# Optimization experiments

Measured on AMD Instinct MI355X. Metric: run time of the kernel, lower is better.

## Reference

```python
import jax, jax.numpy as jnp
import numpy as np

B, TQ, TK = 4, 256, 256
Q, K, H = 256, 256, 256


def setup_inputs() -> dict:
    key = jax.random.key(0)
    ks = jax.random.split(key, 10)
    s = 0.05
    return {
        "queries": jax.random.normal(ks[0], (B, TQ, Q), dtype=jnp.float32),
        "keys": jax.random.normal(ks[1], (B, TK, K), dtype=jnp.float32),
        # lengths in [T//2, T] so no fully-masked query rows (torch would NaN there too)
        "query_lengths": jax.random.randint(ks[2], (B,), TQ // 2, TQ + 1),
        "key_lengths": jax.random.randint(ks[3], (B,), TK // 2, TK + 1),
        # nn.Linear(Q+K, H): weight applied as x @ W1; torch concat order is [keys, queries]
        "W1": jax.random.normal(ks[4], (K + Q, H), dtype=jnp.float32) * s,
        "b1": jax.random.normal(ks[5], (H,), dtype=jnp.float32) * s,
        "W2": jax.random.normal(ks[6], (H, H), dtype=jnp.float32) * s,
        "b2": jax.random.normal(ks[7], (H,), dtype=jnp.float32) * s,
        "W3": jax.random.normal(ks[8], (H, 1), dtype=jnp.float32) * s,
        "b3": jax.random.normal(ks[9], (1,), dtype=jnp.float32) * s,
    }


def reference(queries, keys, query_lengths, key_lengths, W1, b1, W2, b2, W3, b3):
    Bn, Tq, Qd = queries.shape
    Tk, Kd = keys.shape[1], keys.shape[2]
    # Split the first linear: concat([keys, queries]) @ W1 == keys@W1[:K] + queries@W1[K:]
    kh = jnp.einsum("bkd,dh->bkh", keys, W1[:Kd])      # [B,Tk,H]
    qh = jnp.einsum("bqd,dh->bqh", queries, W1[Kd:])   # [B,Tq,H]
    h = jax.nn.relu(qh[:, :, None, :] + kh[:, None, :, :] + b1)  # [B,Tq,Tk,H]
    h = jax.nn.relu(jnp.einsum("bqkh,hg->bqkg", h, W2) + b2)     # [B,Tq,Tk,H]
    scores = jnp.einsum("bqkh,h->bqk", h, W3[:, 0]) + b3[0]       # [B,Tq,Tk]
    # mask True where position is padding (query OR key out of range)
    mask = (jnp.arange(Tq)[None, :, None] >= query_lengths[:, None, None]) | (
        jnp.arange(Tk)[None, None, :] >= key_lengths[:, None, None]
    )
    scores = jnp.where(mask, -1e30, scores)
    probs = jax.nn.softmax(scores, axis=-1)
    probs = jnp.where(mask, 0.0, probs)
    return jnp.einsum("bqk,bkd->bqd", probs, keys)  # [B,Tq,K]
```

## Files before the change

### kernel.cpp

```cpp
#include <hip/hip_runtime.h>
#include <cstdint>

#define BATCH 4
#define TQ 256
#define TK 256
#define DIM 256
#define HD 256

typedef _Float16 f16x8 __attribute__((ext_vector_type(8)));
typedef float f32x4 __attribute__((ext_vector_type(4)));

union U4H8 { uint4 u; f16x8 v; };

__device__ __forceinline__ unsigned short f2h(float f) {
    _Float16 h = (_Float16)f;
    unsigned short u;
    __builtin_memcpy(&u, &h, 2);
    return u;
}

__device__ __forceinline__ float h2f(unsigned short u) {
    _Float16 h;
    __builtin_memcpy(&h, &u, 2);
    return (float)h;
}

__device__ __forceinline__ uint32_t pk2h(float a, float b) {
    auto r = __builtin_amdgcn_cvt_pkrtz(a, b);
    uint32_t w;
    __builtin_memcpy(&w, &r, 4);
    return w;
}

__global__ __launch_bounds__(256) void pack(
    const float* __restrict__ queries, const float* __restrict__ keys,
    const float* __restrict__ W1, const float* __restrict__ W2,
    unsigned short* __restrict__ Xh, unsigned short* __restrict__ Xl,
    unsigned short* __restrict__ W1Th, unsigned short* __restrict__ W1Tl,
    unsigned short* __restrict__ W2T) {
    int i = blockIdx.x;
    int t = threadIdx.x;
    if (i < 512) {
        const float* src = (i < 256 ? queries : keys) + (((i & 255) * 256 + t) << 2);
        float4 v = *(const float4*)src;
        uint32_t h0 = pk2h(v.x, v.y), h1 = pk2h(v.z, v.w);
        float f0 = h2f((unsigned short)h0), f1 = h2f((unsigned short)(h0 >> 16));
        float f2 = h2f((unsigned short)h1), f3 = h2f((unsigned short)(h1 >> 16));
        uint32_t l0 = pk2h(v.x - f0, v.y - f1), l1 = pk2h(v.z - f2, v.w - f3);
        int o = i * 256 + t;
        ((uint2*)Xh)[o] = make_uint2(h0, h1);
        ((uint2*)Xl)[o] = make_uint2(l0, l1);
        return;
    }
    __shared__ float tile[32][33];
    int tx = t & 31, ty = t >> 5;
    if (i < 640) {
        int bi = i - 512;
        int kt = (bi >> 3) * 32, nt = (bi & 7) * 32;
#pragma unroll
        for (int r = 0; r < 4; ++r)
            tile[ty + r * 8][tx] = W1[(kt + ty + r * 8) * HD + nt + tx];
        __syncthreads();
#pragma unroll
        for (int r = 0; r < 4; ++r) {
            float v = tile[tx][ty + r * 8];
            unsigned short h = f2h(v);
            int o = (nt + ty + r * 8) * 512 + kt + tx;
            W1Th[o] = h;
            W1Tl[o] = f2h(v - h2f(h));
        }
        return;
    }
    int bi = i - 640;
    int tc = (bi & 7) * 32, tn = (bi >> 3) * 32;
#pragma unroll
    for (int r = 0; r < 4; ++r)
        tile[ty + r * 8][tx] = W2[(tc + ty + r * 8) * HD + tn + tx];
    __syncthreads();
#pragma unroll
    for (int r = 0; r < 4; ++r)
        W2T[(tn + ty + r * 8) * HD + tc + tx] = f2h(tile[tx][ty + r * 8]);
}

__global__ __launch_bounds__(256) void prep_mfma(
    const unsigned short* __restrict__ Xh, const unsigned short* __restrict__ Xl,
    const unsigned short* __restrict__ W1Th, const unsigned short* __restrict__ W1Tl,
    const float* __restrict__ b1, float* __restrict__ qkh) {
    int mblk = blockIdx.x >> 2, nblk = blockIdx.x & 3;
    int t = threadIdx.x, wid = t >> 6, lane = t & 63;
    int col = lane & 15, quad = lane >> 4;
    int arow = mblk * 64 + wid * 16 + col;
    bool isQ = mblk < 16;
    int koff = isQ ? 256 : 0;

    const uint4* axh = (const uint4*)(Xh + arow * DIM) + quad;
    const uint4* axl = (const uint4*)(Xl + arow * DIM) + quad;
    const uint4* pbh[4];
    const uint4* pbl[4];
    float b1v[4];
#pragma unroll
    for (int nt = 0; nt < 4; ++nt) {
        int n = nblk * 64 + nt * 16 + col;
        pbh[nt] = (const uint4*)(W1Th + n * 512 + koff) + quad;
        pbl[nt] = (const uint4*)(W1Tl + n * 512 + koff) + quad;
        b1v[nt] = isQ ? b1[n] : 0.f;
    }
    f32x4 acc[4] = {};
#pragma unroll
    for (int s = 0; s < 8; ++s) {
        U4H8 ah, al;
        ah.u = axh[s * 4];
        al.u = axl[s * 4];
#pragma unroll
        for (int nt = 0; nt < 4; ++nt) {
            U4H8 bh, bl;
            bh.u = pbh[nt][s * 4];
            bl.u = pbl[nt][s * 4];
            acc[nt] = __builtin_amdgcn_mfma_f32_16x16x32_f16(ah.v, bh.v, acc[nt], 0, 0, 0);
            acc[nt] = __builtin_amdgcn_mfma_f32_16x16x32_f16(al.v, bh.v, acc[nt], 0, 0, 0);
            acc[nt] = __builtin_amdgcn_mfma_f32_16x16x32_f16(ah.v, bl.v, acc[nt], 0, 0, 0);
        }
    }
#pragma unroll
    for (int nt = 0; nt < 4; ++nt)
#pragma unroll
        for (int r = 0; r < 4; ++r)
            qkh[(mblk * 64 + wid * 16 + quad * 4 + r) * HD + nblk * 64 + nt * 16 + col] =
                acc[nt][r] + b1v[nt];
}

__global__ __launch_bounds__(256, 3) void mlp_attn(
    const float* __restrict__ qh, const float* __restrict__ kh,
    const unsigned short* __restrict__ W2T,
    const float* __restrict__ b2, const float* __restrict__ W3,
    const float* __restrict__ keys,
    const int* __restrict__ qlens, const int* __restrict__ klens,
    float* __restrict__ out) {
    int bid = blockIdx.x;
    int b = bid >> 8;
    int q = bid & 255;
    int t = threadIdx.x;
    float* orow = out + (b * TQ + q) * DIM;
    if (q >= qlens[b]) { orow[t] = 0.f; return; }
    int klen = klens[b];
    int nch = (klen + 63) >> 6;

    __shared__ uint4 Afrag[8][4][64];
    __shared__ float srow[TK];
    __shared__ float red[8];

    int wid = t >> 6, lane = t & 63;
    int col = lane & 15, quad = lane >> 4;

    int nb = wid * 64;
    const uint4* w2r[4];
    float b2v[4], w3v[4];
#pragma unroll
    for (int nt = 0; nt < 4; ++nt) {
        int n = nb + nt * 16 + col;
        w2r[nt] = (const uint4*)(W2T + n * HD) + quad;
        b2v[nt] = b2[n];
        w3v[nt] = W3[n];
    }

    int p = (wid << 4) | col;
    const float* qrow = qh + (b * TQ + q) * HD + quad * 8;
    const float* kbase = kh + (b * TK) * HD + quad * 8;

    srow[t] = 0.f;

    for (int c = 0; c < nch; ++c) {
        if (c) __syncthreads();
        {
            const float* krow = kbase + (c * 64 + p) * HD;
            uint4* dst = &Afrag[0][wid][lane];
#pragma unroll 2
            for (int s = 0; s < 8; ++s) {
                const float4 k0 = *(const float4*)(krow + s * 32);
                const float4 k1 = *(const float4*)(krow + s * 32 + 4);
                const float4 q0 = *(const float4*)(qrow + s * 32);
                const float4 q1 = *(const float4*)(qrow + s * 32 + 4);
                uint4 w;
                w.x = pk2h(fmaxf(k0.x + q0.x, 0.f), fmaxf(k0.y + q0.y, 0.f));
                w.y = pk2h(fmaxf(k0.z + q0.z, 0.f), fmaxf(k0.w + q0.w, 0.f));
                w.z = pk2h(fmaxf(k1.x + q1.x, 0.f), fmaxf(k1.y + q1.y, 0.f));
                w.w = pk2h(fmaxf(k1.z + q1.z, 0.f), fmaxf(k1.w + q1.w, 0.f));
                dst[s * 256] = w;
            }
        }
        __syncthreads();

        f32x4 acc[4][4] = {};
        uint4 bst[2][4];
#pragma unroll
        for (int nt = 0; nt < 4; ++nt) bst[0][nt] = w2r[nt][0];
#pragma unroll
        for (int s = 0; s < 8; ++s) {
            int pp = s & 1;
            if (s < 7) {
#pragma unroll
                for (int nt = 0; nt < 4; ++nt)
                    bst[pp ^ 1][nt] = w2r[nt][(s + 1) * 4];
            }
#pragma unroll
            for (int mt = 0; mt < 4; ++mt) {
                U4H8 au;
                au.u = Afrag[s][mt][lane];
#pragma unroll
                for (int nt = 0; nt < 4; ++nt) {
                    U4H8 bu;
                    bu.u = bst[pp][nt];
                    acc[mt][nt] = __builtin_amdgcn_mfma_f32_16x16x32_f16(
                        au.v, bu.v, acc[mt][nt], 0, 0, 0);
                }
            }
        }

#pragma unroll
        for (int mt = 0; mt < 4; ++mt) {
            float part[4];
#pragma unroll
            for (int r = 0; r < 4; ++r) {
                float pa = 0.f;
#pragma unroll
                for (int nt = 0; nt < 4; ++nt)
                    pa = fmaf(fmaxf(acc[mt][nt][r] + b2v[nt], 0.f), w3v[nt], pa);
                part[r] = pa;
            }
#pragma unroll
            for (int off = 1; off < 16; off <<= 1)
#pragma unroll
                for (int r = 0; r < 4; ++r)
                    part[r] += __shfl_xor(part[r], off, 64);
            if (col == 0)
#pragma unroll
                for (int r = 0; r < 4; ++r)
                    atomicAdd(&srow[c * 64 + mt * 16 + quad * 4 + r], part[r]);
        }
    }
    __syncthreads();

    float s = (t < klen) ? srow[t] : -3.4e38f;
    float m = s;
#pragma unroll
    for (int off = 1; off < 64; off <<= 1) m = fmaxf(m, __shfl_xor(m, off, 64));
    if (lane == 0) red[wid] = m;
    __syncthreads();
    m = fmaxf(fmaxf(red[0], red[1]), fmaxf(red[2], red[3]));
    float e = (t < klen) ? __expf(s - m) : 0.f;
    float sum = e;
#pragma unroll
    for (int off = 1; off < 64; off <<= 1) sum += __shfl_xor(sum, off, 64);
    if (lane == 0) red[4 + wid] = sum;
    __syncthreads();
    float denom = red[4] + red[5] + red[6] + red[7];
    srow[t] = e / denom;
    __syncthreads();

    float acc = 0.f;
    const float* kp = keys + b * TK * DIM + t;
#pragma unroll 16
    for (int k = 0; k < klen; ++k) acc = fmaf(srow[k], kp[k * DIM], acc);
    orow[t] = acc;
}

extern "C" void kernel_launch(void* const* d_in, const int* in_sizes, int n_in,
                              void* d_out, int out_size, void* d_ws, size_t ws_size,
                              hipStream_t stream) {
    (void)in_sizes; (void)n_in; (void)out_size; (void)ws_size;
    const float* queries = (const float*)d_in[0];
    const float* keys    = (const float*)d_in[1];
    const int*   qlens   = (const int*)d_in[2];
    const int*   klens   = (const int*)d_in[3];
    const float* W1      = (const float*)d_in[4];
    const float* b1      = (const float*)d_in[5];
    const float* W2      = (const float*)d_in[6];
    const float* b2      = (const float*)d_in[7];
    const float* W3      = (const float*)d_in[8];
    float* out = (float*)d_out;

    float* qkh = (float*)d_ws;
    float* qh = qkh;
    float* kh = qkh + 1024 * HD;
    unsigned short* Xh   = (unsigned short*)(qkh + 2048 * HD);
    unsigned short* Xl   = Xh + 2048 * DIM;
    unsigned short* W1Th = Xl + 2048 * DIM;
    unsigned short* W1Tl = W1Th + 256 * 512;
    unsigned short* W2T  = W1Tl + 256 * 512;

    pack<<<704, 256, 0, stream>>>(queries, keys, W1, W2, Xh, Xl, W1Th, W1Tl, W2T);
    prep_mfma<<<128, 256, 0, stream>>>(Xh, Xl, W1Th, W1Tl, b1, qkh);
    mlp_attn<<<BATCH * TQ, 256, 0, stream>>>(
        qh, kh, W2T, b2, W3, keys, qlens, klens, out);
}
```

Before: 153.9 us.

## Split MLP scoring and P·V into separate kernels with wider blocks

The fused per-query kernel is split in two. The first kernel computes the masked softmax probabilities with 512-thread blocks: each wave now covers 32 output columns of W2 instead of 64, and the A-fragment fill is spread across twice as many waves. Probabilities are written to workspace. A second kernel computes probs·keys for four query rows per block, so each key element read is reused four times. The intent is higher MFMA occupancy and less redundant key traffic, at the cost of an extra launch and a round trip of the probability matrix through global memory.

```diff
diff --git a/kernel.cpp b/kernel.cpp
--- a/kernel.cpp
+++ b/kernel.cpp
@@ -129,57 +129,56 @@
                 acc[nt][r] + b1v[nt];
 }
 
-__global__ __launch_bounds__(256, 3) void mlp_attn(
+__global__ __launch_bounds__(512, 4) void mlp_scores(
     const float* __restrict__ qh, const float* __restrict__ kh,
     const unsigned short* __restrict__ W2T,
     const float* __restrict__ b2, const float* __restrict__ W3,
-    const float* __restrict__ keys,
     const int* __restrict__ qlens, const int* __restrict__ klens,
-    float* __restrict__ out) {
+    float* __restrict__ probs) {
     int bid = blockIdx.x;
     int b = bid >> 8;
     int q = bid & 255;
     int t = threadIdx.x;
-    float* orow = out + (b * TQ + q) * DIM;
-    if (q >= qlens[b]) { orow[t] = 0.f; return; }
+    if (q >= qlens[b]) return;
     int klen = klens[b];
     int nch = (klen + 63) >> 6;
 
     __shared__ uint4 Afrag[8][4][64];
     __shared__ float srow[TK];
-    __shared__ float red[8];
-
-    int wid = t >> 6, lane = t & 63;
+    __shared__ float redm[8], reds[8];
+
+    int wv = t >> 6, lane = t & 63;
     int col = lane & 15, quad = lane >> 4;
 
-    int nb = wid * 64;
-    const uint4* w2r[4];
-    float b2v[4], w3v[4];
-#pragma unroll
-    for (int nt = 0; nt < 4; ++nt) {
-        int n = nb + nt * 16 + col;
+    const uint4* w2r[2];
+    float b2v[2], w3v[2];
+#pragma unroll
+    for (int nt = 0; nt < 2; ++nt) {
+        int n = wv * 32 + nt * 16 + col;
         w2r[nt] = (const uint4*)(W2T + n * HD) + quad;
         b2v[nt] = b2[n];
         w3v[nt] = W3[n];
     }
 
-    int p = (wid << 4) | col;
+    int mt_s = wv & 3, s0 = (wv >> 2) << 2;
+    int p = (mt_s << 4) | col;
     const float* qrow = qh + (b * TQ + q) * HD + quad * 8;
     const float* kbase = kh + (b * TK) * HD + quad * 8;
 
-    srow[t] = 0.f;
+    if (t < TK) srow[t] = 0.f;
 
     for (int c = 0; c < nch; ++c) {
         if (c) __syncthreads();
         {
             const float* krow = kbase + (c * 64 + p) * HD;
-            uint4* dst = &Afrag[0][wid][lane];
+            uint4* dst = &Afrag[s0][mt_s][lane];
 #pragma unroll 2
-            for (int s = 0; s < 8; ++s) {
-                const float4 k0 = *(const float4*)(krow + s * 32);
-                const float4 k1 = *(const float4*)(krow + s * 32 + 4);
-                const float4 q0 = *(const float4*)(qrow + s * 32);
-                const float4 q1 = *(const float4*)(qrow + s * 32 + 4);
+            for (int s = 0; s < 4; ++s) {
+                int c0 = (s0 + s) * 32;
+                const float4 k0 = *(const float4*)(krow + c0);
+                const float4 k1 = *(const float4*)(krow + c0 + 4);
+                const float4 q0 = *(const float4*)(qrow + c0);
+                const float4 q1 = *(const float4*)(qrow + c0 + 4);
                 uint4 w;
                 w.x = pk2h(fmaxf(k0.x + q0.x, 0.f), fmaxf(k0.y + q0.y, 0.f));
                 w.y = pk2h(fmaxf(k0.z + q0.z, 0.f), fmaxf(k0.w + q0.w, 0.f));
@@ -190,16 +189,16 @@
         }
         __syncthreads();
 
-        f32x4 acc[4][4] = {};
-        uint4 bst[2][4];
-#pragma unroll
-        for (int nt = 0; nt < 4; ++nt) bst[0][nt] = w2r[nt][0];
+        f32x4 acc[4][2] = {};
+        uint4 bst[2][2];
+#pragma unroll
+        for (int nt = 0; nt < 2; ++nt) bst[0][nt] = w2r[nt][0];
 #pragma unroll
         for (int s = 0; s < 8; ++s) {
             int pp = s & 1;
             if (s < 7) {
 #pragma unroll
-                for (int nt = 0; nt < 4; ++nt)
+                for (int nt = 0; nt < 2; ++nt)
                     bst[pp ^ 1][nt] = w2r[nt][(s + 1) * 4];
             }
 #pragma unroll
@@ -207,7 +206,7 @@
                 U4H8 au;
                 au.u = Afrag[s][mt][lane];
 #pragma unroll
-                for (int nt = 0; nt < 4; ++nt) {
+                for (int nt = 0; nt < 2; ++nt) {
                     U4H8 bu;
                     bu.u = bst[pp][nt];
                     acc[mt][nt] = __builtin_amdgcn_mfma_f32_16x16x32_f16(
@@ -223,7 +222,7 @@
             for (int r = 0; r < 4; ++r) {
                 float pa = 0.f;
 #pragma unroll
-                for (int nt = 0; nt < 4; ++nt)
+                for (int nt = 0; nt < 2; ++nt)
                     pa = fmaf(fmaxf(acc[mt][nt][r] + b2v[nt], 0.f), w3v[nt], pa);
                 part[r] = pa;
             }
@@ -244,24 +243,44 @@
     float m = s;
 #pragma unroll
     for (int off = 1; off < 64; off <<= 1) m = fmaxf(m, __shfl_xor(m, off, 64));
-    if (lane == 0) red[wid] = m;
-    __syncthreads();
-    m = fmaxf(fmaxf(red[0], red[1]), fmaxf(red[2], red[3]));
+    if (lane == 0) redm[wv] = m;
+    __syncthreads();
+    m = fmaxf(fmaxf(redm[0], redm[1]), fmaxf(redm[2], redm[3]));
     float e = (t < klen) ? __expf(s - m) : 0.f;
     float sum = e;
 #pragma unroll
     for (int off = 1; off < 64; off <<= 1) sum += __shfl_xor(sum, off, 64);
-    if (lane == 0) red[4 + wid] = sum;
-    __syncthreads();
-    float denom = red[4] + red[5] + red[6] + red[7];
-    srow[t] = e / denom;
-    __syncthreads();
-
-    float acc = 0.f;
+    if (lane == 0) reds[wv] = sum;
+    __syncthreads();
+    float denom = reds[0] + reds[1] + reds[2] + reds[3];
+    if (t < TK) probs[(b * TQ + q) * TK + t] = e / denom;
+}
+
+__global__ __launch_bounds__(256) void pv(
+    const float* __restrict__ probs, const float* __restrict__ keys,
+    const int* __restrict__ qlens, const int* __restrict__ klens,
+    float* __restrict__ out) {
+    int bid = blockIdx.x;
+    int b = bid >> 6, qg = (bid & 63) * 4;
+    int t = threadIdx.x;
+    int qlen = qlens[b], klen = klens[b];
+    __shared__ float pl[4][TK];
+#pragma unroll
+    for (int r = 0; r < 4; ++r) {
+        int q = qg + r;
+        pl[r][t] = (q < qlen) ? probs[(b * TQ + q) * TK + t] : 0.f;
+    }
+    __syncthreads();
+    float acc[4] = {0.f, 0.f, 0.f, 0.f};
     const float* kp = keys + b * TK * DIM + t;
-#pragma unroll 16
-    for (int k = 0; k < klen; ++k) acc = fmaf(srow[k], kp[k * DIM], acc);
-    orow[t] = acc;
+#pragma unroll 8
+    for (int k = 0; k < klen; ++k) {
+        float kv = kp[k * DIM];
+#pragma unroll
+        for (int r = 0; r < 4; ++r) acc[r] = fmaf(pl[r][k], kv, acc[r]);
+    }
+#pragma unroll
+    for (int r = 0; r < 4; ++r) out[(b * TQ + qg + r) * DIM + t] = acc[r];
 }
 
 extern "C" void kernel_launch(void* const* d_in, const int* in_sizes, int n_in,
@@ -287,9 +306,11 @@
     unsigned short* W1Th = Xl + 2048 * DIM;
     unsigned short* W1Tl = W1Th + 256 * 512;
     unsigned short* W2T  = W1Tl + 256 * 512;
+    float* probs = (float*)(W2T + 256 * HD);
 
     pack<<<704, 256, 0, stream>>>(queries, keys, W1, W2, Xh, Xl, W1Th, W1Tl, W2T);
     prep_mfma<<<128, 256, 0, stream>>>(Xh, Xl, W1Th, W1Tl, b1, qkh);
-    mlp_attn<<<BATCH * TQ, 256, 0, stream>>>(
-        qh, kh, W2T, b2, W3, keys, qlens, klens, out);
-}
+    mlp_scores<<<BATCH * TQ, 512, 0, stream>>>(
+        qh, kh, W2T, b2, W3, qlens, klens, probs);
+    pv<<<BATCH * (TQ / 4), 256, 0, stream>>>(probs, keys, qlens, klens, out);
+}
```

After: 163.9 us. +6.5%, slower.
